# Kernel optimization log

Hardware: AMD Instinct MI355X
Metric: run time of the kernel (lower is better)

Reference implementation:

```python
import jax, jax.numpy as jnp
import numpy as np

EPS = 1e-8


def setup_inputs() -> dict:
    key = jax.random.key(0)
    ks = jax.random.split(key, 6)
    N, H, B = 1000000, 256, 1024
    x = jax.random.normal(ks[0], (N, H), dtype=jnp.float32)
    W1 = jax.random.normal(ks[1], (H, H // 2), dtype=jnp.float32) * (1.0 / np.sqrt(H))
    b1 = jax.random.normal(ks[2], (H // 2,), dtype=jnp.float32) * 0.01
    W2 = jax.random.normal(ks[3], (H // 2, 1), dtype=jnp.float32) * (1.0 / np.sqrt(H // 2))
    b2 = jax.random.normal(ks[4], (1,), dtype=jnp.float32) * 0.01
    batch = jnp.sort(jax.random.randint(ks[5], (N,), 0, B, dtype=jnp.int64))
    return {"x": x, "W1": W1, "b1": b1, "W2": W2, "b2": b2,
            "batch": batch, "batch_size": B}


def reference(x, W1, b1, W2, b2, batch, batch_size):
    # attention MLP: Linear -> Tanh -> Linear -> softmax over all nodes (dim 0)
    scores = jnp.tanh(x @ W1 + b1) @ W2 + b2          # [N, 1]
    w = jax.nn.softmax(scores, axis=0)[:, 0]           # [N]
    # per-graph normalization (segment sums replace the dense one-hot mask)
    seg_sum = jax.ops.segment_sum(w, batch, num_segments=batch_size)  # [B]
    w_norm = w / (seg_sum[batch] + EPS)                # [N]
    # weighted per-graph feature aggregation
    graph_embedding = jax.ops.segment_sum(w_norm[:, None] * x, batch,
                                          num_segments=batch_size)   # [B, H]
    return graph_embedding
```

## Files before the change

kernel.cpp:

```cpp
#include <hip/hip_runtime.h>
#include <hip/hip_bf16.h>
#include <cstdint>


#define H_DIM 256
#define HID   128
#define CHUNK 64
#define XT_STRIDE 264

typedef _Float16 half8 __attribute__((ext_vector_type(8)));
typedef _Float16 half4 __attribute__((ext_vector_type(4)));
typedef float floatx4 __attribute__((ext_vector_type(4)));

__device__ __forceinline__ float fast_tanh(float y) {
    float e2 = __expf(2.0f * y);
    return 1.0f - 2.0f / (e2 + 1.0f);
}

__global__ void prep_w1(const float* __restrict__ W1, _Float16* __restrict__ w1h) {
    int idx = blockIdx.x * blockDim.x + threadIdx.x;
    if (idx >= 8 * 8 * 64 * 8) return;
    int j  = idx & 7;
    int l  = (idx >> 3) & 63;
    int ks = (idx >> 9) & 7;
    int nt = idx >> 12;
    int k = ks * 32 + ((l >> 4) << 3) + j;
    int n = nt * 16 + (l & 15);
    w1h[idx] = (_Float16)W1[k * HID + n];
}

__global__ __launch_bounds__(256, 4) void fused_kernel(
    const float* __restrict__ x, const _Float16* __restrict__ w1h,
    const float* __restrict__ b1, const float* __restrict__ W2,
    const float* __restrict__ b2, const int* __restrict__ batch,
    float* __restrict__ out, int N)
{
    __shared__ __align__(16) _Float16 xt[CHUNK * XT_STRIDE];
    __shared__ float pbuf[4][CHUNK];
    __shared__ float wbuf[CHUNK];
    __shared__ float fz[2];

    int tid = threadIdx.x, b = blockIdx.x;
    int wave = tid >> 6, lane = tid & 63, g = lane >> 4, c = lane & 15;

    int lo = 0, hi = N;
    while (lo < hi) { int mid = (lo + hi) >> 1; if (batch[mid] < b) lo = mid + 1; else hi = mid; }
    int start = lo; hi = N;
    while (lo < hi) { int mid = (lo + hi) >> 1; if (batch[mid] <= b) lo = mid + 1; else hi = mid; }
    int end = lo;
    int seglen = end - start;
    if (seglen <= 0) { out[(size_t)b * H_DIM + tid] = 0.0f; return; }

    half8 bfr[2][8];
#pragma unroll
    for (int nt2 = 0; nt2 < 2; ++nt2)
#pragma unroll
        for (int ks = 0; ks < 8; ++ks)
            bfr[nt2][ks] = *(const half8*)&w1h[(((2 * wave + nt2) * 8 + ks) * 64 + lane) * 8];

    float b1r[2], w2r[2];
#pragma unroll
    for (int nt2 = 0; nt2 < 2; ++nt2) {
        b1r[nt2] = b1[(2 * wave + nt2) * 16 + c];
        w2r[nt2] = W2[(2 * wave + nt2) * 16 + c];
    }
    float b2v = b2[0];

    float m_run = -3.0e38f;
    float Zrun  = 0.0f;
    float accv  = 0.0f;

    for (int co = 0; co < seglen; co += CHUNK) {
        int cnt = min(CHUNK, seglen - co);

        __syncthreads();

#pragma unroll
        for (int hb = 0; hb < 2; ++hb) {
            float4 rv[8];
#pragma unroll
            for (int i = 0; i < 8; ++i) {
                int fi = tid + (hb * 8 + i) * 256;
                int row = fi >> 6, col4 = fi & 63;
                int rr = row < cnt ? row : cnt - 1;
                rv[i] = *(const float4*)(x + (size_t)(start + co + rr) * H_DIM + col4 * 4);
            }
#pragma unroll
            for (int i = 0; i < 8; ++i) {
                int fi = tid + (hb * 8 + i) * 256;
                int row = fi >> 6, col4 = fi & 63;
                half4 hv;
                hv[0] = (_Float16)rv[i].x; hv[1] = (_Float16)rv[i].y;
                hv[2] = (_Float16)rv[i].z; hv[3] = (_Float16)rv[i].w;
                *(half4*)&xt[row * XT_STRIDE + col4 * 4] = hv;
            }
        }

        __syncthreads();

        floatx4 acc[4][2];
#pragma unroll
        for (int mt = 0; mt < 4; ++mt)
#pragma unroll
            for (int nt2 = 0; nt2 < 2; ++nt2)
#pragma unroll
                for (int q = 0; q < 4; ++q) acc[mt][nt2][q] = 0.0f;

#pragma unroll
        for (int ks = 0; ks < 8; ++ks) {
#pragma unroll
            for (int mt = 0; mt < 4; ++mt) {
                half8 af = *(const half8*)&xt[(mt * 16 + c) * XT_STRIDE + ks * 32 + g * 8];
                acc[mt][0] = __builtin_amdgcn_mfma_f32_16x16x32_f16(af, bfr[0][ks], acc[mt][0], 0, 0, 0);
                acc[mt][1] = __builtin_amdgcn_mfma_f32_16x16x32_f16(af, bfr[1][ks], acc[mt][1], 0, 0, 0);
            }
        }

#pragma unroll
        for (int mt = 0; mt < 4; ++mt) {
#pragma unroll
            for (int r = 0; r < 4; ++r) {
                float p = fast_tanh(acc[mt][0][r] + b1r[0]) * w2r[0]
                        + fast_tanh(acc[mt][1][r] + b1r[1]) * w2r[1];
                p += __shfl_xor(p, 8);
                p += __shfl_xor(p, 4);
                p += __shfl_xor(p, 2);
                p += __shfl_xor(p, 1);
                if (c == 0) pbuf[wave][mt * 16 + g * 4 + r] = p;
            }
        }

        __syncthreads();

        if (wave == 0) {
            float sv = (lane < cnt)
                ? (pbuf[0][lane] + pbuf[1][lane] + pbuf[2][lane] + pbuf[3][lane] + b2v)
                : -3.0e38f;
            float cm = sv;
#pragma unroll
            for (int off = 32; off; off >>= 1) cm = fmaxf(cm, __shfl_xor(cm, off));
            float m_new = fmaxf(m_run, cm);
            float f = __expf(m_run - m_new);
            float w = __expf(sv - m_new);
            wbuf[lane] = w;
            float sw = w;
#pragma unroll
            for (int off = 32; off; off >>= 1) sw += __shfl_xor(sw, off);
            Zrun = Zrun * f + sw;
            m_run = m_new;
            if (lane == 0) fz[0] = f;
        }

        __syncthreads();

        float f = fz[0];
        float a = 0.0f;
#pragma unroll 8
        for (int j = 0; j < CHUNK; ++j)
            a = fmaf(wbuf[j], (float)xt[j * XT_STRIDE + tid], a);
        accv = accv * f + a;
    }

    if (tid == 0) fz[1] = Zrun;
    __syncthreads();
    out[(size_t)b * H_DIM + tid] = accv / fz[1];
}

extern "C" void kernel_launch(void* const* d_in, const int* in_sizes, int n_in,
                              void* d_out, int out_size, void* d_ws, size_t ws_size,
                              hipStream_t stream) {
    const float* x    = (const float*)d_in[0];
    const float* W1   = (const float*)d_in[1];
    const float* b1   = (const float*)d_in[2];
    const float* W2   = (const float*)d_in[3];
    const float* b2   = (const float*)d_in[4];
    const int*   batch = (const int*)d_in[5];
    int N = in_sizes[5];
    int B = out_size / H_DIM;

    _Float16* w1h = (_Float16*)d_ws;

    prep_w1<<<32768 / 256, 256, 0, stream>>>(W1, w1h);
    fused_kernel<<<B, 256, 0, stream>>>(x, w1h, b1, W2, b2, batch, (float*)d_out, N);
}
```

Before: 396.7 us.

## Stream W1 fragments per k-step, vectorize aggregation with 8-wide column groups

Stops holding all W1 MFMA fragments in registers and reloads them from global/L2 on each k-step, which lowers register pressure. The x load stage is split into four smaller batches of float4 loads. The weighted aggregation now has each thread handle 8 columns over 8 rows using half8 LDS reads, instead of one column over 64 rows with scalar reads, and the partial sums are reduced across row groups through shared memory at the end. In exchange it adds repeated W1 global loads on every chunk and an extra reduction step.

```diff
diff --git a/kernel.cpp b/kernel.cpp
--- a/kernel.cpp
+++ b/kernel.cpp
@@ -42,6 +42,7 @@
 
     int tid = threadIdx.x, b = blockIdx.x;
     int wave = tid >> 6, lane = tid & 63, g = lane >> 4, c = lane & 15;
+    int colg = tid & 31, rowg = tid >> 5;
 
     int lo = 0, hi = N;
     while (lo < hi) { int mid = (lo + hi) >> 1; if (batch[mid] < b) lo = mid + 1; else hi = mid; }
@@ -50,13 +51,6 @@
     int end = lo;
     int seglen = end - start;
     if (seglen <= 0) { out[(size_t)b * H_DIM + tid] = 0.0f; return; }
-
-    half8 bfr[2][8];
-#pragma unroll
-    for (int nt2 = 0; nt2 < 2; ++nt2)
-#pragma unroll
-        for (int ks = 0; ks < 8; ++ks)
-            bfr[nt2][ks] = *(const half8*)&w1h[(((2 * wave + nt2) * 8 + ks) * 64 + lane) * 8];
 
     float b1r[2], w2r[2];
 #pragma unroll
@@ -68,7 +62,9 @@
 
     float m_run = -3.0e38f;
     float Zrun  = 0.0f;
-    float accv  = 0.0f;
+    float a[8];
+#pragma unroll
+    for (int k2 = 0; k2 < 8; ++k2) a[k2] = 0.0f;
 
     for (int co = 0; co < seglen; co += CHUNK) {
         int cnt = min(CHUNK, seglen - co);
@@ -76,18 +72,18 @@
         __syncthreads();
 
 #pragma unroll
-        for (int hb = 0; hb < 2; ++hb) {
-            float4 rv[8];
+        for (int bb = 0; bb < 4; ++bb) {
+            float4 rv[4];
 #pragma unroll
-            for (int i = 0; i < 8; ++i) {
-                int fi = tid + (hb * 8 + i) * 256;
+            for (int i = 0; i < 4; ++i) {
+                int fi = tid + (bb * 4 + i) * 256;
                 int row = fi >> 6, col4 = fi & 63;
                 int rr = row < cnt ? row : cnt - 1;
                 rv[i] = *(const float4*)(x + (size_t)(start + co + rr) * H_DIM + col4 * 4);
             }
 #pragma unroll
-            for (int i = 0; i < 8; ++i) {
-                int fi = tid + (hb * 8 + i) * 256;
+            for (int i = 0; i < 4; ++i) {
+                int fi = tid + (bb * 4 + i) * 256;
                 int row = fi >> 6, col4 = fi & 63;
                 half4 hv;
                 hv[0] = (_Float16)rv[i].x; hv[1] = (_Float16)rv[i].y;
@@ -106,13 +102,16 @@
 #pragma unroll
                 for (int q = 0; q < 4; ++q) acc[mt][nt2][q] = 0.0f;
 
+        const half8* bbase = (const half8*)&w1h[((2 * wave * 8) * 64 + lane) * 8];
 #pragma unroll
         for (int ks = 0; ks < 8; ++ks) {
+            half8 bf0 = bbase[ks * 64];
+            half8 bf1 = bbase[(8 + ks) * 64];
 #pragma unroll
             for (int mt = 0; mt < 4; ++mt) {
                 half8 af = *(const half8*)&xt[(mt * 16 + c) * XT_STRIDE + ks * 32 + g * 8];
-                acc[mt][0] = __builtin_amdgcn_mfma_f32_16x16x32_f16(af, bfr[0][ks], acc[mt][0], 0, 0, 0);
-                acc[mt][1] = __builtin_amdgcn_mfma_f32_16x16x32_f16(af, bfr[1][ks], acc[mt][1], 0, 0, 0);
+                acc[mt][0] = __builtin_amdgcn_mfma_f32_16x16x32_f16(af, bf0, acc[mt][0], 0, 0, 0);
+                acc[mt][1] = __builtin_amdgcn_mfma_f32_16x16x32_f16(af, bf1, acc[mt][1], 0, 0, 0);
             }
         }
 
@@ -154,16 +153,30 @@
         __syncthreads();
 
         float f = fz[0];
-        float a = 0.0f;
-#pragma unroll 8
-        for (int j = 0; j < CHUNK; ++j)
-            a = fmaf(wbuf[j], (float)xt[j * XT_STRIDE + tid], a);
-        accv = accv * f + a;
+#pragma unroll
+        for (int k2 = 0; k2 < 8; ++k2) a[k2] *= f;
+#pragma unroll
+        for (int i = 0; i < 8; ++i) {
+            int j = rowg + 8 * i;
+            float w = wbuf[j];
+            half8 hx = *(const half8*)&xt[j * XT_STRIDE + colg * 8];
+#pragma unroll
+            for (int k2 = 0; k2 < 8; ++k2)
+                a[k2] = fmaf((float)hx[k2], w, a[k2]);
+        }
     }
 
     if (tid == 0) fz[1] = Zrun;
+
     __syncthreads();
-    out[(size_t)b * H_DIM + tid] = accv / fz[1];
+    float* scr = (float*)xt;
+    *(float4*)&scr[rowg * 256 + colg * 8]     = make_float4(a[0], a[1], a[2], a[3]);
+    *(float4*)&scr[rowg * 256 + colg * 8 + 4] = make_float4(a[4], a[5], a[6], a[7]);
+    __syncthreads();
+    float r = 0.0f;
+#pragma unroll
+    for (int i = 0; i < 8; ++i) r += scr[i * 256 + tid];
+    out[(size_t)b * H_DIM + tid] = r / fz[1];
 }
 
 extern "C" void kernel_launch(void* const* d_in, const int* in_sizes, int n_in,
```

After: 398.7 us. About the same (+0.5%).
